# Performance work log

Measured on AMD Instinct MI355X. Metric: run time of the kernel, lower is better.

Reference implementation:

```python
import jax, jax.numpy as jnp
import numpy as np

N_NODES = 100000
N_EDGES = 1600000
F_IN = 128
HID = 128
LAT = 64
NUM_LAYERS = 3
NUM_GRAPHS = 512


def setup_inputs() -> dict:
    key = jax.random.key(0)
    ks = jax.random.split(key, 12)
    x = jax.random.normal(ks[0], (N_NODES, F_IN), dtype=jnp.float32)
    edge_index = jax.random.randint(ks[1], (2, N_EDGES), 0, N_NODES, dtype=jnp.int64)
    batch = jnp.sort(jax.random.randint(ks[2], (N_NODES,), 0, NUM_GRAPHS, dtype=jnp.int32))
    s_in = 1.0 / np.sqrt(F_IN)
    s_h = 1.0 / np.sqrt(HID)
    W_in = jax.random.uniform(ks[3], (F_IN, HID), jnp.float32, -s_in, s_in)
    b_in = jax.random.uniform(ks[4], (HID,), jnp.float32, -s_in, s_in)
    W_msg = jax.random.uniform(ks[5], (NUM_LAYERS, HID, HID), jnp.float32, -s_h, s_h)
    b_msg = jax.random.uniform(ks[6], (NUM_LAYERS, HID), jnp.float32, -s_h, s_h)
    W_upd = jax.random.uniform(ks[7], (NUM_LAYERS, HID, HID), jnp.float32, -s_h, s_h)
    b_upd = jax.random.uniform(ks[8], (NUM_LAYERS, HID), jnp.float32, -s_h, s_h)
    W_mean = jax.random.uniform(ks[9], (HID, LAT), jnp.float32, -s_h, s_h)
    b_mean = jax.random.uniform(ks[10], (LAT,), jnp.float32, -s_h, s_h)
    W_logvar = jax.random.uniform(ks[11], (HID, LAT), jnp.float32, -s_h, s_h)
    b_logvar = jax.random.uniform(jax.random.fold_in(key, 99), (LAT,), jnp.float32, -s_h, s_h)
    return {"x": x, "edge_index": edge_index, "batch": batch,
            "W_in": W_in, "b_in": b_in, "W_msg": W_msg, "b_msg": b_msg,
            "W_upd": W_upd, "b_upd": b_upd, "W_mean": W_mean, "b_mean": b_mean,
            "W_logvar": W_logvar, "b_logvar": b_logvar}


def _mp_layer(h, src, dst, Wm, bm, Wu, bu):
    # message: Linear+ReLU on all nodes, gather per-edge, scatter-add into dst
    messages = jax.nn.relu(h @ Wm + bm)                      # [N, H]
    agg = jax.ops.segment_sum(messages[src], dst, num_segments=N_NODES)  # [N, H]
    return jax.nn.relu(agg @ Wu + bu) + h                    # update + residual


def reference(x, edge_index, batch, W_in, b_in, W_msg, b_msg, W_upd, b_upd,
              W_mean, b_mean, W_logvar, b_logvar):
    src = edge_index[0]
    dst = edge_index[1]
    h = jax.nn.relu(x @ W_in + b_in)
    for l in range(NUM_LAYERS):
        h = _mp_layer(h, src, dst, W_msg[l], b_msg[l], W_upd[l], b_upd[l])
    # graph-level sum pooling by batch segment ids
    g = jax.ops.segment_sum(h, batch, num_segments=NUM_GRAPHS)  # [G, H]
    z_mean = g @ W_mean + b_mean
    z_logvar = g @ W_logvar + b_logvar
    return (z_mean, z_logvar)
```

## Files before the change

kernel.cpp:

```cpp
#include <hip/hip_runtime.h>
#include <hip/hip_bf16.h>
#include <cstdint>

#define N_NODES 100000
#define N_EDGES 1600000
#define N_GRAPHS 512
#define N_LAYERS 3
#define NB 1563
#define BCAP 2048
#define NFB 256

typedef __bf16 bf16x8 __attribute__((ext_vector_type(8)));
typedef float f32x4 __attribute__((ext_vector_type(4)));
typedef uint uint4v __attribute__((ext_vector_type(4)));

__device__ __forceinline__ float bf2f(ushort u) {
  uint v = ((uint)u) << 16;
  return __builtin_bit_cast(float, v);
}
__device__ __forceinline__ ushort f2bf(float f) {
  uint u = __builtin_bit_cast(uint, f);
  u += 0x7FFF + ((u >> 16) & 1);
  return (ushort)(u >> 16);
}
__device__ __forceinline__ uint pk2(float lo, float hi) {
  return (uint)f2bf(lo) | ((uint)f2bf(hi) << 16);
}

struct BsortSh {
  uint sp[BCAP];
  uint so[BCAP];
  int cnt[64], pref[64], cur[64];
};
struct GemmSh {
  ushort sA[64][136];
  int sb[64];
};
union FatSh {
  BsortSh b;
  GemmSh g;
};

__device__ __forceinline__ void bsort_body(BsortSh& S, int bk, int t,
    const int* __restrict__ bcur, const uint* __restrict__ packed,
    uint* __restrict__ srcs, int* __restrict__ nbeg, int* __restrict__ nend) {
  const int c = min(bcur[bk * 16], BCAP);
  if (t < 64) S.cnt[t] = 0;
  __syncthreads();
  for (int i = t; i < c; i += 256) {
    uint p = packed[(size_t)bk * BCAP + i];
    S.sp[i] = p;
    atomicAdd(&S.cnt[p >> 17], 1);
  }
  __syncthreads();
  if (t == 0) {
    int run = 0;
    #pragma unroll
    for (int j = 0; j < 64; ++j) { S.pref[j] = run; run += S.cnt[j]; }
  }
  if (t < 64) S.cur[t] = 0;
  __syncthreads();
  for (int i = t; i < c; i += 256) {
    uint p = S.sp[i];
    int n = p >> 17;
    int pos = atomicAdd(&S.cur[n], 1);
    S.so[S.pref[n] + pos] = min(p & 0x1FFFF, (uint)(N_NODES - 1));
  }
  __syncthreads();
  for (int i = t; i < c; i += 256) srcs[(size_t)bk * BCAP + i] = S.so[i];
  if (t < 64) {
    int base = bk * BCAP;
    nbeg[bk * 64 + t] = base + S.pref[t];
    nend[bk * 64 + t] = base + S.pref[t] + S.cnt[t];
  }
}

template <bool CVT, bool RES, bool SECOND, bool POOL>
__device__ __forceinline__ void gemm2_body(GemmSh& S, int row0, int t,
    const ushort* __restrict__ Ab, const float* __restrict__ Af,
    const ushort* __restrict__ W1, const float* __restrict__ b1,
    const ushort* __restrict__ res, ushort* __restrict__ out1,
    const ushort* __restrict__ W2, const float* __restrict__ b2,
    ushort* __restrict__ out2,
    const int* __restrict__ batch, float* __restrict__ g) {
  const int lane = t & 63;
  const int col0 = (t >> 6) * 32;
  const int lr = lane & 15, lk = (lane >> 4) * 8;

  bf16x8 bfr[4][2];
  #pragma unroll
  for (int kk = 0; kk < 4; ++kk) {
    bfr[kk][0] = *(const bf16x8*)&W1[(col0 + lr) * 128 + kk * 32 + lk];
    bfr[kk][1] = *(const bf16x8*)&W1[(col0 + 16 + lr) * 128 + kk * 32 + lk];
  }

  #pragma unroll
  for (int i = 0; i < 4; ++i) {
    int c = t + 256 * i;
    int r = c >> 4, k8 = (c & 15) * 8;
    int gr = min(row0 + r, N_NODES - 1);
    if (CVT) {
      const float* src = &Af[(size_t)gr * 128 + k8];
      float4 x0 = *(const float4*)src;
      float4 x1 = *(const float4*)(src + 4);
      uint4v u;
      u.x = pk2(x0.x, x0.y); u.y = pk2(x0.z, x0.w);
      u.z = pk2(x1.x, x1.y); u.w = pk2(x1.z, x1.w);
      *(uint4v*)&S.sA[r][k8] = u;
    } else {
      *(uint4*)&S.sA[r][k8] = *(const uint4*)&Ab[(size_t)gr * 128 + k8];
    }
  }
  __syncthreads();

  f32x4 acc[4][2] = {};
  #pragma unroll
  for (int kk = 0; kk < 4; ++kk) {
    int kb = kk * 32 + lk;
    #pragma unroll
    for (int m = 0; m < 4; ++m) {
      bf16x8 a = *(const bf16x8*)&S.sA[m * 16 + lr][kb];
      acc[m][0] = __builtin_amdgcn_mfma_f32_16x16x32_bf16(a, bfr[kk][0], acc[m][0], 0, 0, 0);
      acc[m][1] = __builtin_amdgcn_mfma_f32_16x16x32_bf16(a, bfr[kk][1], acc[m][1], 0, 0, 0);
    }
  }

  bf16x8 bfr2[4][2];
  if (SECOND) {
    #pragma unroll
    for (int kk = 0; kk < 4; ++kk) {
      bfr2[kk][0] = *(const bf16x8*)&W2[(col0 + lr) * 128 + kk * 32 + lk];
      bfr2[kk][1] = *(const bf16x8*)&W2[(col0 + 16 + lr) * 128 + kk * 32 + lk];
    }
  }
  __syncthreads();

  const int rb = (lane >> 4) * 4;
  #pragma unroll
  for (int n = 0; n < 2; ++n) {
    int col = col0 + n * 16 + lr;
    float bv = b1[col];
    #pragma unroll
    for (int m = 0; m < 4; ++m) {
      #pragma unroll
      for (int j = 0; j < 4; ++j) {
        int r = row0 + m * 16 + rb + j;
        float v = fmaxf(acc[m][n][j] + bv, 0.f);
        if (RES && r < N_NODES) v += bf2f(res[(size_t)r * 128 + col]);
        S.sA[m * 16 + rb + j][col] = f2bf(v);
      }
    }
  }
  if (POOL && t < 64)
    S.sb[t] = (row0 + t < N_NODES) ? batch[row0 + t] : -1;
  __syncthreads();

  if (POOL) {
    int c = t & 127, half = t >> 7;
    int v0 = half * 32, v1 = v0 + 32;
    int cur = S.sb[v0];
    if (cur >= 0) {
      float acc2 = 0.f;
      for (int v = v0; v < v1; ++v) {
        int b = S.sb[v];
        if (b < 0) break;
        if (b != cur) {
          unsafeAtomicAdd(&g[cur * 128 + c], acc2);
          acc2 = 0.f;
          cur = b;
        }
        acc2 += bf2f(S.sA[v][c]);
      }
      unsafeAtomicAdd(&g[cur * 128 + c], acc2);
    }
    return;
  }

  #pragma unroll
  for (int i = 0; i < 4; ++i) {
    int c = t + 256 * i;
    int r = c >> 4, k8 = (c & 15) * 8;
    int gr = row0 + r;
    if (gr < N_NODES)
      *(uint4*)&out1[(size_t)gr * 128 + k8] = *(const uint4*)&S.sA[r][k8];
  }

  if (SECOND) {
    f32x4 acc2[4][2] = {};
    #pragma unroll
    for (int kk = 0; kk < 4; ++kk) {
      int kb = kk * 32 + lk;
      #pragma unroll
      for (int m = 0; m < 4; ++m) {
        bf16x8 a = *(const bf16x8*)&S.sA[m * 16 + lr][kb];
        acc2[m][0] = __builtin_amdgcn_mfma_f32_16x16x32_bf16(a, bfr2[kk][0], acc2[m][0], 0, 0, 0);
        acc2[m][1] = __builtin_amdgcn_mfma_f32_16x16x32_bf16(a, bfr2[kk][1], acc2[m][1], 0, 0, 0);
      }
    }
    __syncthreads();

    #pragma unroll
    for (int n = 0; n < 2; ++n) {
      int col = col0 + n * 16 + lr;
      float bv = b2[col];
      #pragma unroll
      for (int m = 0; m < 4; ++m) {
        #pragma unroll
        for (int j = 0; j < 4; ++j) {
          float v = fmaxf(acc2[m][n][j] + bv, 0.f);
          S.sA[m * 16 + rb + j][col] = f2bf(v);
        }
      }
    }
    __syncthreads();

    #pragma unroll
    for (int i = 0; i < 4; ++i) {
      int c = t + 256 * i;
      int r = c >> 4, k8 = (c & 15) * 8;
      int gr = row0 + r;
      if (gr < N_NODES)
        *(uint4*)&out2[(size_t)gr * 128 + k8] = *(const uint4*)&S.sA[r][k8];
    }
  }
}

__global__ __launch_bounds__(1024) void k_bfill_prep(const int* __restrict__ e32,
    const long long* __restrict__ e64, int* __restrict__ bcur,
    uint* __restrict__ packed,
    const float* __restrict__ W_in, const float* __restrict__ W_msg,
    const float* __restrict__ W_upd, ushort* __restrict__ Wt) {
  __shared__ int lcnt[NB];
  __shared__ int lbase[NB];
  __shared__ int sflag;
  const int t = threadIdx.x;

  if (blockIdx.x >= NFB) {
    int b = blockIdx.x - NFB;
    const float* W = (b == 0) ? W_in : (b <= 3 ? W_msg + (size_t)(b - 1) * 16384
                                               : W_upd + (size_t)(b - 4) * 16384);
    ushort* O = Wt + (size_t)b * 16384;
    for (int i = t; i < 16384; i += 1024) {
      int k = i >> 7, c = i & 127;
      O[c * 128 + k] = f2bf(W[i]);
    }
    return;
  }

  const int e0 = blockIdx.x * (N_EDGES / NFB);
  const int e1 = e0 + (N_EDGES / NFB);
  for (int k = t; k < NB; k += 1024) lcnt[k] = 0;
  if (t == 0) {
    int any = 0;
    for (int i = 1; i < 128; i += 2) any |= e32[i];
    sflag = (any == 0) ? 1 : 0;
  }
  __syncthreads();
  const bool f64 = (sflag != 0);
  if (f64) {
    for (int i = e0 + t; i < e1; i += 1024)
      atomicAdd(&lcnt[((int)e64[N_EDGES + i]) >> 6], 1);
  } else {
    for (int i = e0 + t; i < e1; i += 1024)
      atomicAdd(&lcnt[e32[N_EDGES + i] >> 6], 1);
  }
  __syncthreads();
  for (int k = t; k < NB; k += 1024) {
    int c = lcnt[k];
    lbase[k] = (c > 0) ? atomicAdd(&bcur[k * 16], c) : 0;
    lcnt[k] = 0;
  }
  __syncthreads();
  for (int i = e0 + t; i < e1; i += 1024) {
    int d, s;
    if (f64) { d = (int)e64[N_EDGES + i]; s = (int)e64[i]; }
    else     { d = e32[N_EDGES + i];      s = e32[i]; }
    int bk = d >> 6;
    int pos = lbase[bk] + atomicAdd(&lcnt[bk], 1);
    if (pos < BCAP)
      packed[(size_t)bk * BCAP + pos] = ((uint)(d & 63) << 17) | (uint)s;
  }
}

__global__ __launch_bounds__(256) void k_bsort_gemm(const int* __restrict__ bcur,
    const uint* __restrict__ packed, uint* __restrict__ srcs,
    int* __restrict__ nbeg, int* __restrict__ nend,
    const float* __restrict__ x, const ushort* __restrict__ Wt,
    const float* __restrict__ b_in, ushort* __restrict__ h0,
    const ushort* __restrict__ Wm0, const float* __restrict__ bm0,
    ushort* __restrict__ msg0) {
  __shared__ FatSh sh;
  if (blockIdx.x < NB) {
    bsort_body(sh.b, blockIdx.x, threadIdx.x, bcur, packed, srcs, nbeg, nend);
  } else {
    gemm2_body<true, false, true, false>(sh.g, (blockIdx.x - NB) * 64,
        threadIdx.x, nullptr, x, Wt, b_in, nullptr, h0, Wm0, bm0, msg0,
        nullptr, nullptr);
  }
}

template <bool CVT, bool RES, bool SECOND, bool POOL>
__global__ __launch_bounds__(256) void k_gemm2(const ushort* __restrict__ Ab,
    const float* __restrict__ Af,
    const ushort* __restrict__ W1, const float* __restrict__ b1,
    const ushort* __restrict__ res, ushort* __restrict__ out1,
    const ushort* __restrict__ W2, const float* __restrict__ b2,
    ushort* __restrict__ out2,
    const int* __restrict__ batch, float* __restrict__ g) {
  __shared__ GemmSh sh;
  gemm2_body<CVT, RES, SECOND, POOL>(sh, blockIdx.x * 64, threadIdx.x,
      Ab, Af, W1, b1, res, out1, W2, b2, out2, batch, g);
}

__global__ __launch_bounds__(256) void k_aggregate(const int* __restrict__ nbeg,
    const int* __restrict__ nend, const uint* __restrict__ srcs,
    const ushort* __restrict__ msg, ushort* __restrict__ agg) {
  int wid = blockIdx.x * 4 + (threadIdx.x >> 6);
  if (wid >= N_NODES) return;
  const int lane = threadIdx.x & 63;
  const uint sub = lane >> 4, l16 = lane & 15;
  int e = nbeg[wid];
  const int en = nend[wid];
  float a[8] = {0.f, 0.f, 0.f, 0.f, 0.f, 0.f, 0.f, 0.f};

#define ACC8(mv)                                              \
  a[0] += bf2f((ushort)mv.x); a[1] += bf2f((ushort)(mv.x >> 16)); \
  a[2] += bf2f((ushort)mv.y); a[3] += bf2f((ushort)(mv.y >> 16)); \
  a[4] += bf2f((ushort)mv.z); a[5] += bf2f((ushort)(mv.z >> 16)); \
  a[6] += bf2f((ushort)mv.w); a[7] += bf2f((ushort)(mv.w >> 16));

  for (; e + 16 <= en; e += 16) {
    uint s0 = srcs[e + sub];
    uint s1 = srcs[e + 4 + sub];
    uint s2 = srcs[e + 8 + sub];
    uint s3 = srcs[e + 12 + sub];
    uint4 m0 = *(const uint4*)&msg[s0 * 128u + l16 * 8u];
    uint4 m1 = *(const uint4*)&msg[s1 * 128u + l16 * 8u];
    uint4 m2 = *(const uint4*)&msg[s2 * 128u + l16 * 8u];
    uint4 m3 = *(const uint4*)&msg[s3 * 128u + l16 * 8u];
    ACC8(m0) ACC8(m1) ACC8(m2) ACC8(m3)
  }
  const uint rem = (uint)(en - e);
  #pragma unroll
  for (uint k = 0; k < 4; ++k) {
    uint idx = k * 4 + sub;
    if (idx < rem) {
      uint s = srcs[e + idx];
      uint4 m = *(const uint4*)&msg[s * 128u + l16 * 8u];
      ACC8(m)
    }
  }
#undef ACC8

  #pragma unroll
  for (int j = 0; j < 8; ++j) {
    a[j] += __shfl_xor(a[j], 16, 64);
    a[j] += __shfl_xor(a[j], 32, 64);
  }
  if (sub == 0) {
    uint4 r;
    r.x = pk2(a[0], a[1]);
    r.y = pk2(a[2], a[3]);
    r.z = pk2(a[4], a[5]);
    r.w = pk2(a[6], a[7]);
    *(uint4*)&agg[(size_t)wid * 128 + l16 * 8] = r;
  }
}

__global__ __launch_bounds__(128) void k_head(const float* __restrict__ g,
    const float* __restrict__ Wm, const float* __restrict__ bm,
    const float* __restrict__ Wl, const float* __restrict__ bl,
    float* __restrict__ out) {
  __shared__ float sg[128];
  int gr = blockIdx.x, t = threadIdx.x;
  sg[t] = g[gr * 128 + t];
  __syncthreads();
  const float* W = (t < 64) ? Wm : Wl;
  const float* b = (t < 64) ? bm : bl;
  int c = t & 63;
  float acc = b[c];
  #pragma unroll 8
  for (int k = 0; k < 128; ++k) acc += sg[k] * W[k * 64 + c];
  out[(size_t)(t < 64 ? 0 : N_GRAPHS * 64) + (size_t)gr * 64 + c] = acc;
}

extern "C" void kernel_launch(void* const* d_in, const int* in_sizes, int n_in,
                              void* d_out, int out_size, void* d_ws, size_t ws_size,
                              hipStream_t stream) {
  const float* x      = (const float*)d_in[0];
  const int* e32      = (const int*)d_in[1];
  const long long* e64 = (const long long*)d_in[1];
  const int* batch    = (const int*)d_in[2];
  const float* W_in   = (const float*)d_in[3];
  const float* b_in   = (const float*)d_in[4];
  const float* W_msg  = (const float*)d_in[5];
  const float* b_msg  = (const float*)d_in[6];
  const float* W_upd  = (const float*)d_in[7];
  const float* b_upd  = (const float*)d_in[8];
  const float* W_mean = (const float*)d_in[9];
  const float* b_mean = (const float*)d_in[10];
  const float* W_lv   = (const float*)d_in[11];
  const float* b_lv   = (const float*)d_in[12];
  float* out = (float*)d_out;

  char* p = (char*)d_ws;
  auto alloc = [&](size_t bytes) {
    char* r = p;
    p += (bytes + 255) & ~(size_t)255;
    return r;
  };
  ushort* bufA   = (ushort*)alloc((size_t)N_NODES * 128 * 2);
  ushort* bufB   = (ushort*)alloc((size_t)N_NODES * 128 * 2);
  ushort* bufC   = (ushort*)alloc((size_t)N_NODES * 128 * 2);
  ushort* bufM   = (ushort*)alloc((size_t)N_NODES * 128 * 2);
  ushort* Wt     = (ushort*)alloc((size_t)7 * 16384 * 2);
  uint*   packed = (uint*)alloc((size_t)NB * BCAP * 4);
  uint*   srcs   = (uint*)alloc((size_t)NB * BCAP * 4);
  int*    bcur   = (int*)alloc((size_t)NB * 16 * 4);
  int*    nbeg   = (int*)alloc((size_t)NB * 64 * 4);
  int*    nend   = (int*)alloc((size_t)NB * 64 * 4);
  float*  g      = (float*)alloc((size_t)N_GRAPHS * 128 * 4);

  hipMemsetAsync(bcur, 0, (size_t)NB * 16 * 4, stream);
  hipMemsetAsync(g, 0, (size_t)N_GRAPHS * 128 * 4, stream);

  const ushort* Wm[3] = {Wt + 16384, Wt + 2 * 16384, Wt + 3 * 16384};
  const ushort* Wu[3] = {Wt + 4 * 16384, Wt + 5 * 16384, Wt + 6 * 16384};

  k_bfill_prep<<<NFB + 7, 1024, 0, stream>>>(e32, e64, bcur, packed,
                                             W_in, W_msg, W_upd, Wt);

  k_bsort_gemm<<<2 * NB, 256, 0, stream>>>(bcur, packed, srcs, nbeg, nend,
                                           x, Wt, b_in, bufA, Wm[0], b_msg, bufM);

  ushort* h = bufA;
  ushort* hn = bufB;
  for (int l = 0; l < N_LAYERS; ++l) {
    k_aggregate<<<(N_NODES + 3) / 4, 256, 0, stream>>>(nbeg, nend, srcs, bufM, bufC);
    if (l < N_LAYERS - 1) {
      k_gemm2<false, true, true, false><<<NB, 256, 0, stream>>>(
          bufC, nullptr, Wu[l], b_upd + (size_t)l * 128, h, hn,
          Wm[l + 1], b_msg + (size_t)(l + 1) * 128, bufM, nullptr, nullptr);
      ushort* sw = h; h = hn; hn = sw;
    } else {
      k_gemm2<false, true, false, true><<<NB, 256, 0, stream>>>(
          bufC, nullptr, Wu[l], b_upd + (size_t)l * 128, h, nullptr,
          nullptr, nullptr, nullptr, batch, g);
    }
  }

  k_head<<<N_GRAPHS, 128, 0, stream>>>(g, W_mean, b_mean, W_lv, b_lv, out);
}
```

Measured before the change: 385.2 us.

## Split aggregation across column groups with edges spread over lane pairs

Remaps the gather-sum aggregation so each block handles one 16-column slice of four nodes, with lane pairs covering 32 edges in parallel per wave. This aims to expose more memory-level parallelism and more blocks for latency hiding. In exchange, each gather becomes a 32-byte access, edge indices are re-read by eight blocks, and the cross-lane reduction grows to five shuffle steps. With about 16 edges per node, many lanes sit idle.

```diff
diff --git a/kernel.cpp b/kernel.cpp
--- a/kernel.cpp
+++ b/kernel.cpp
@@ -315,55 +315,42 @@
 __global__ __launch_bounds__(256) void k_aggregate(const int* __restrict__ nbeg,
     const int* __restrict__ nend, const uint* __restrict__ srcs,
     const ushort* __restrict__ msg, ushort* __restrict__ agg) {
-  int wid = blockIdx.x * 4 + (threadIdx.x >> 6);
+  const int b = blockIdx.x;
+  const int cg = b & 7;
+  const int wid = (b >> 3) * 4 + (threadIdx.x >> 6);
   if (wid >= N_NODES) return;
   const int lane = threadIdx.x & 63;
-  const uint sub = lane >> 4, l16 = lane & 15;
+  const uint half = lane & 1;
+  const int esub = lane >> 1;
+  const uint colbase = cg * 16u + half * 8u;
   int e = nbeg[wid];
   const int en = nend[wid];
   float a[8] = {0.f, 0.f, 0.f, 0.f, 0.f, 0.f, 0.f, 0.f};
 
-#define ACC8(mv)                                              \
-  a[0] += bf2f((ushort)mv.x); a[1] += bf2f((ushort)(mv.x >> 16)); \
-  a[2] += bf2f((ushort)mv.y); a[3] += bf2f((ushort)(mv.y >> 16)); \
-  a[4] += bf2f((ushort)mv.z); a[5] += bf2f((ushort)(mv.z >> 16)); \
-  a[6] += bf2f((ushort)mv.w); a[7] += bf2f((ushort)(mv.w >> 16));
-
-  for (; e + 16 <= en; e += 16) {
-    uint s0 = srcs[e + sub];
-    uint s1 = srcs[e + 4 + sub];
-    uint s2 = srcs[e + 8 + sub];
-    uint s3 = srcs[e + 12 + sub];
-    uint4 m0 = *(const uint4*)&msg[s0 * 128u + l16 * 8u];
-    uint4 m1 = *(const uint4*)&msg[s1 * 128u + l16 * 8u];
-    uint4 m2 = *(const uint4*)&msg[s2 * 128u + l16 * 8u];
-    uint4 m3 = *(const uint4*)&msg[s3 * 128u + l16 * 8u];
-    ACC8(m0) ACC8(m1) ACC8(m2) ACC8(m3)
-  }
-  const uint rem = (uint)(en - e);
-  #pragma unroll
-  for (uint k = 0; k < 4; ++k) {
-    uint idx = k * 4 + sub;
-    if (idx < rem) {
-      uint s = srcs[e + idx];
-      uint4 m = *(const uint4*)&msg[s * 128u + l16 * 8u];
-      ACC8(m)
-    }
-  }
-#undef ACC8
-
-  #pragma unroll
-  for (int j = 0; j < 8; ++j) {
-    a[j] += __shfl_xor(a[j], 16, 64);
-    a[j] += __shfl_xor(a[j], 32, 64);
-  }
-  if (sub == 0) {
+  for (; e < en; e += 32) {
+    int idx = e + esub;
+    if (idx < en) {
+      uint s = srcs[idx];
+      uint4 m = *(const uint4*)&msg[s * 128u + colbase];
+      a[0] += bf2f((ushort)m.x); a[1] += bf2f((ushort)(m.x >> 16));
+      a[2] += bf2f((ushort)m.y); a[3] += bf2f((ushort)(m.y >> 16));
+      a[4] += bf2f((ushort)m.z); a[5] += bf2f((ushort)(m.z >> 16));
+      a[6] += bf2f((ushort)m.w); a[7] += bf2f((ushort)(m.w >> 16));
+    }
+  }
+
+  #pragma unroll
+  for (int off = 2; off < 64; off <<= 1) {
+    #pragma unroll
+    for (int j = 0; j < 8; ++j) a[j] += __shfl_xor(a[j], off, 64);
+  }
+  if (esub == 0) {
     uint4 r;
     r.x = pk2(a[0], a[1]);
     r.y = pk2(a[2], a[3]);
     r.z = pk2(a[4], a[5]);
     r.w = pk2(a[6], a[7]);
-    *(uint4*)&agg[(size_t)wid * 128 + l16 * 8] = r;
+    *(uint4*)&agg[wid * 128u + colbase] = r;
   }
 }
 
@@ -433,10 +420,12 @@
   k_bsort_gemm<<<2 * NB, 256, 0, stream>>>(bcur, packed, srcs, nbeg, nend,
                                            x, Wt, b_in, bufA, Wm[0], b_msg, bufM);
 
+  const int AGG_GRID = ((N_NODES + 3) / 4) * 8;
+
   ushort* h = bufA;
   ushort* hn = bufB;
   for (int l = 0; l < N_LAYERS; ++l) {
-    k_aggregate<<<(N_NODES + 3) / 4, 256, 0, stream>>>(nbeg, nend, srcs, bufM, bufC);
+    k_aggregate<<<AGG_GRID, 256, 0, stream>>>(nbeg, nend, srcs, bufM, bufC);
     if (l < N_LAYERS - 1) {
       k_gemm2<false, true, true, false><<<NB, 256, 0, stream>>>(
           bufC, nullptr, Wu[l], b_upd + (size_t)l * 128, h, hn,
```

After: 1.173 ms. 3.04x slower.
